# Kernel tuning notes

Measured on AMD Instinct MI355X. Metric: run time of the kernel, lower is better.

## Reference

```python
import jax, jax.numpy as jnp
import numpy as np
from math import sqrt

B, L, S, H, E, D = 2, 2048, 2048, 8, 64, 64


def setup_inputs() -> dict:
    key = jax.random.key(0)
    kq, kk, kv, kb = jax.random.split(key, 4)
    queries = jax.random.normal(kq, (B, L, H, E), dtype=jnp.float32)
    keys = jax.random.normal(kk, (B, S, H, E), dtype=jnp.float32)
    values = jax.random.normal(kv, (B, S, H, D), dtype=jnp.float32)
    # TriangularCausalMask: True above the diagonal (positions to mask)
    causal = jnp.triu(jnp.ones((L, S), dtype=bool), k=1)
    attn_mask = jnp.broadcast_to(causal[None, None], (B, 1, L, S))
    attn_bias = jax.random.normal(kb, (B, L, S, H), dtype=jnp.float32) * 0.1
    return {"queries": queries, "keys": keys, "values": values,
            "attn_mask": attn_mask, "attn_bias": attn_bias}


def reference(queries, keys, values, attn_mask, attn_bias):
    scale = 1.0 / sqrt(E)
    # scores: [B, H, L, S]
    scores = jnp.einsum('blhe,bshe->bhls', queries, keys)
    scores = jnp.where(attn_mask, -jnp.inf, scores)
    bias = jnp.transpose(attn_bias, (0, 3, 1, 2))  # [B,H,L,S]
    A = jax.nn.softmax(scores * scale + bias, axis=-1)  # dropout = identity (eval)
    V = jnp.einsum('bhls,bshd->blhd', A, values)
    return V
```

## Files before the change

kernel.cpp:

```cpp
#include <hip/hip_runtime.h>
#include <stdint.h>

#define Bb 2
#define Ll 2048
#define Ss 2048
#define Hh 8
#define Ee 64
#define Dd 64

#define LOG2E 1.4426950408889634f
#define QSCALE (0.125f * LOG2E)
#define NEG_BIG (-1e30f)
#define QT_ELEMS 2097152

typedef short bf16x8 __attribute__((ext_vector_type(8)));
typedef short bf16x4 __attribute__((ext_vector_type(4)));
typedef float f32x4  __attribute__((ext_vector_type(4)));

__device__ __forceinline__ short f2bf(float f) {
  uint32_t u = __float_as_uint(f);
  u += 0x7fffu + ((u >> 16) & 1u);
  return (short)(u >> 16);
}
__device__ __forceinline__ float bf2f(short s) {
  return __uint_as_float(((uint32_t)(unsigned short)s) << 16);
}
__device__ __forceinline__ f32x4 mfma_pv(bf16x4 a, bf16x4 b, f32x4 c) {
#if __has_builtin(__builtin_amdgcn_mfma_f32_16x16x16_bf16)
  return __builtin_amdgcn_mfma_f32_16x16x16_bf16(a, b, c, 0, 0, 0);
#else
  return __builtin_amdgcn_mfma_f32_16x16x16bf16_1k(a, b, c, 0, 0, 0);
#endif
}

#define BLOCK_SYNC() do {                                   \
    asm volatile("s_waitcnt lgkmcnt(0)" ::: "memory");      \
    __builtin_amdgcn_s_barrier();                           \
    asm volatile("" ::: "memory");                          \
  } while (0)

__global__ __launch_bounds__(256)
void prep_qkv(const float* __restrict__ Q, const float* __restrict__ K,
              const float* __restrict__ V, short* __restrict__ Qt,
              short* __restrict__ Kt, short* __restrict__ Vt)
{
  const int blk = blockIdx.x;
  const int tid = threadIdx.x;
  if (blk < 1024) {
    const int c = tid & 15;
    #pragma unroll
    for (int pass = 0; pass < 4; ++pass) {
      const int rowg = blk * 64 + pass * 16 + (tid >> 4);
      const int tensor = rowg >> 15;
      const int r2 = rowg & 32767;
      const float* src = (tensor ? K : Q) + (size_t)r2 * 64 + c * 4;
      const float4 v = *(const float4*)(src);
      const int b = r2 >> 14, l = (r2 >> 3) & 2047, hh = r2 & 7;
      const float sc = tensor ? 1.0f : QSCALE;
      bf16x4 o;
      o[0] = f2bf(v.x * sc); o[1] = f2bf(v.y * sc);
      o[2] = f2bf(v.z * sc); o[3] = f2bf(v.w * sc);
      short* dst = (tensor ? Kt : Qt) + ((size_t)((b * 8 + hh) * 2048 + l)) * 64 + c * 4;
      *reinterpret_cast<bf16x4*>(dst) = o;
    }
  } else {
    const int vb = blk - 1024;
    const int plane = vb >> 5;
    const int b = plane >> 3, hh = plane & 7;
    const int sc = (vb & 31) * 64;
    const int w = tid >> 6, d = tid & 63;
    const int sbase = sc + w * 16;
    const float* src = V + (((size_t)b * Ss + sbase) * Hh + hh) * Dd + d;
    float vals[16];
    #pragma unroll
    for (int i = 0; i < 16; ++i) vals[i] = src[(size_t)i * (Hh * Dd)];
    bf16x8 o0, o1;
    #pragma unroll
    for (int i = 0; i < 8; ++i) { o0[i] = f2bf(vals[i]); o1[i] = f2bf(vals[i + 8]); }
    short* dst = Vt + ((size_t)(plane * 64 + d)) * 2048 + sbase;
    *reinterpret_cast<bf16x8*>(dst)     = o0;
    *reinterpret_cast<bf16x8*>(dst + 8) = o1;
  }
}

__global__ __launch_bounds__(256, 1)
void fattn4(const short* __restrict__ Qt, const short* __restrict__ Kt,
            const short* __restrict__ Vt, const float* __restrict__ Bias,
            float* __restrict__ Out)
{
  __shared__ short Vs[2][4][64][72];
  __shared__ short Bs[2][4][4][16][16];

  const int tid  = threadIdx.x;
  const int wv   = tid >> 6;
  const int lane = tid & 63;
  const int g    = lane >> 4;
  const int n    = lane & 15;

  const int rid    = blockIdx.x;
  const int xcd    = rid & 7;
  const int b      = xcd >> 2;
  const int hhalf  = (xcd >> 1) & 1;
  const int z      = xcd & 1;
  const int pairid = (rid >> 3) * 2 + z;
  const int h      = hhalf * 4 + wv;
  const int p      = b * 8 + h;

  const int sl = tid >> 4;
  const int sq = tid & 15;
  const int srcb = (lane & 48) | ((lane >> 2) & 12);

  for (int job = 0; job < 2; ++job) {
    const int lg = job ? pairid : (127 - pairid);
    const int l0 = lg * 16;
    const int ntiles = (lg >> 2) + 1;
    const int lq = l0 + n;

    const short* qp = Qt + ((size_t)(p * 2048 + l0 + n)) * 64 + g * 8;
    const bf16x8 qf0 = *reinterpret_cast<const bf16x8*>(qp);
    const bf16x8 qf1 = *reinterpret_cast<const bf16x8*>(qp + 32);

    const short* kbase  = Kt + ((size_t)(p * 2048 + n)) * 64 + g * 8;
    const short* vstage = Vt + ((size_t)(p * 64 + lane)) * 2048;
    const float* gb = Bias + (((size_t)(b * Ll + l0 + sl)) * Ss + sq) * Hh + hhalf * 4;

    f32x4 acc[4];
    #pragma unroll
    for (int dt = 0; dt < 4; ++dt) { f32x4 zz = {0.f,0.f,0.f,0.f}; acc[dt] = zz; }
    float m = NEG_BIG, lsum = 0.f;

    bf16x8 kA[4][2], kB[4][2];
    float4 gB0, gB1, gB2, gB3;

#define ISSUE_K(KN, soff) do {                                              \
      const short* kp_ = kbase + (size_t)(soff) * 64;                       \
      _Pragma("unroll")                                                     \
      for (int st_ = 0; st_ < 4; ++st_) {                                   \
        KN[st_][0] = *reinterpret_cast<const bf16x8*>(kp_ + st_ * 16 * 64); \
        KN[st_][1] = *reinterpret_cast<const bf16x8*>(kp_ + st_ * 16 * 64 + 32); \
      }                                                                     \
    } while (0)

#define ISSUE_BIAS(G0, G1, G2, G3, soff) do {                               \
      const float* gp_ = gb + (size_t)(soff) * Hh;                          \
      G0 = *(const float4*)(gp_);                                           \
      G1 = *(const float4*)(gp_ + (size_t)16 * Hh);                         \
      G2 = *(const float4*)(gp_ + (size_t)32 * Hh);                         \
      G3 = *(const float4*)(gp_ + (size_t)48 * Hh);                         \
    } while (0)

#define WRITE_BIAS(buf, G0, G1, G2, G3) do {                                \
      short* w0_ = &Bs[buf][0][0][sl][sq];                                  \
      short* w1_ = &Bs[buf][0][1][sl][sq];                                  \
      short* w2_ = &Bs[buf][0][2][sl][sq];                                  \
      short* w3_ = &Bs[buf][0][3][sl][sq];                                  \
      w0_[0]=f2bf(G0.x*LOG2E); w0_[1024]=f2bf(G0.y*LOG2E); w0_[2048]=f2bf(G0.z*LOG2E); w0_[3072]=f2bf(G0.w*LOG2E); \
      w1_[0]=f2bf(G1.x*LOG2E); w1_[1024]=f2bf(G1.y*LOG2E); w1_[2048]=f2bf(G1.z*LOG2E); w1_[3072]=f2bf(G1.w*LOG2E); \
      w2_[0]=f2bf(G2.x*LOG2E); w2_[1024]=f2bf(G2.y*LOG2E); w2_[2048]=f2bf(G2.z*LOG2E); w2_[3072]=f2bf(G2.w*LOG2E); \
      w3_[0]=f2bf(G3.x*LOG2E); w3_[1024]=f2bf(G3.y*LOG2E); w3_[2048]=f2bf(G3.z*LOG2E); w3_[3072]=f2bf(G3.w*LOG2E); \
    } while (0)

    {
      float4 a0, a1, a2, a3;
      ISSUE_BIAS(a0, a1, a2, a3, 0);
      ISSUE_BIAS(gB0, gB1, gB2, gB3, 64);
      ISSUE_K(kA, 0);
      bf16x8 v0[8];
      #pragma unroll
      for (int c = 0; c < 8; ++c)
        v0[c] = *reinterpret_cast<const bf16x8*>(vstage + c * 8);
      WRITE_BIAS(0, a0, a1, a2, a3);
      #pragma unroll
      for (int c = 0; c < 8; ++c)
        *reinterpret_cast<bf16x8*>(&Vs[0][wv][lane][c * 8]) = v0[c];
    }
    BLOCK_SYNC();

#define TILE(KC, KN, t) do {                                                \
      const int s0_ = (t) * 64;                                             \
      const int cb_ = (t) & 1, nb_ = cb_ ^ 1;                               \
      const bool more1_ = ((t) + 1 < ntiles);                               \
      const bool more2_ = ((t) + 2 < ntiles);                               \
       \
      if (more1_) ISSUE_K(KN, s0_ + 64);                                    \
      bf16x8 vN_[8];                                                        \
      if (more1_) {                                                         \
        _Pragma("unroll")                                                   \
        for (int c = 0; c < 8; ++c)                                         \
          vN_[c] = *reinterpret_cast<const bf16x8*>(vstage + s0_ + 64 + c * 8); \
      }                                                                     \
                                                    \
      f32x4 sacc_[4];                                                       \
      _Pragma("unroll")                                                     \
      for (int st_ = 0; st_ < 4; ++st_) {                                   \
        const bf16x4 bb_ = *reinterpret_cast<const bf16x4*>(&Bs[cb_][wv][st_][n][4 * g]); \
        f32x4 zz_ = {0.f, 0.f, 0.f, 0.f};                                   \
        f32x4 sv_ = __builtin_amdgcn_mfma_f32_16x16x32_bf16(KC[st_][0], qf0, zz_, 0, 0, 0); \
        sv_ = __builtin_amdgcn_mfma_f32_16x16x32_bf16(KC[st_][1], qf1, sv_, 0, 0, 0); \
        const int sb_ = s0_ + st_ * 16 + 4 * g;                             \
        _Pragma("unroll")                                                   \
        for (int r_ = 0; r_ < 4; ++r_)                                      \
          sacc_[st_][r_] = (sb_ + r_ <= lq) ? (sv_[r_] + bf2f(bb_[r_])) : NEG_BIG; \
      }                                                                     \
                                            \
      float tm_ = NEG_BIG;                                                  \
      _Pragma("unroll")                                                     \
      for (int st_ = 0; st_ < 4; ++st_)                                     \
        _Pragma("unroll")                                                   \
        for (int r_ = 0; r_ < 4; ++r_) tm_ = fmaxf(tm_, sacc_[st_][r_]);    \
      tm_ = fmaxf(tm_, __shfl_xor(tm_, 16));                                \
      tm_ = fmaxf(tm_, __shfl_xor(tm_, 32));                                \
      if (__any(tm_ - m > 8.f)) {                                           \
        const float mn_ = fmaxf(m, tm_);                                    \
        const float corr_ = exp2f(m - mn_);                                 \
        m = mn_; lsum *= corr_;                                             \
        const float c0_ = __shfl(corr_, srcb);                              \
        const float c1_ = __shfl(corr_, srcb + 1);                          \
        const float c2_ = __shfl(corr_, srcb + 2);                          \
        const float c3_ = __shfl(corr_, srcb + 3);                          \
        _Pragma("unroll")                                                   \
        for (int dt_ = 0; dt_ < 4; ++dt_) {                                 \
          acc[dt_][0] *= c0_; acc[dt_][1] *= c1_;                           \
          acc[dt_][2] *= c2_; acc[dt_][3] *= c3_;                           \
        }                                                                   \
      }                                                                     \
      bf16x4 pa_[4];                                                        \
      float ps_ = 0.f;                                                      \
      _Pragma("unroll")                                                     \
      for (int st_ = 0; st_ < 4; ++st_) {                                   \
        _Pragma("unroll")                                                   \
        for (int r_ = 0; r_ < 4; ++r_) {                                    \
          const float pe_ = exp2f(sacc_[st_][r_] - m);                      \
          ps_ += pe_;                                                       \
          pa_[st_][r_] = f2bf(pe_);                                         \
        }                                                                   \
      }                                                                     \
      ps_ += __shfl_xor(ps_, 16);                                           \
      ps_ += __shfl_xor(ps_, 32);                                           \
      lsum += ps_;                                                          \
                       \
      _Pragma("unroll")                                                     \
      for (int st_ = 0; st_ < 4; ++st_) {                                   \
        _Pragma("unroll")                                                   \
        for (int dt_ = 0; dt_ < 4; ++dt_) {                                 \
          const bf16x4 vb_ = *reinterpret_cast<const bf16x4*>(              \
              &Vs[cb_][wv][dt_ * 16 + n][st_ * 16 + 4 * g]);                \
          acc[dt_] = mfma_pv(pa_[st_], vb_, acc[dt_]);                      \
        }                                                                   \
      }                                                                     \
                                  \
      if (more1_) {                                                         \
        _Pragma("unroll")                                                   \
        for (int c = 0; c < 8; ++c)                                         \
          *reinterpret_cast<bf16x8*>(&Vs[nb_][wv][lane][c * 8]) = vN_[c];   \
        WRITE_BIAS(nb_, gB0, gB1, gB2, gB3);                                \
      }                                                                     \
      if (more2_) ISSUE_BIAS(gB0, gB1, gB2, gB3, s0_ + 128);                \
      BLOCK_SYNC();                                                         \
    } while (0)

    int t = 0;
    for (;;) {
      TILE(kA, kB, t); if (++t == ntiles) break;
      TILE(kB, kA, t); if (++t == ntiles) break;
    }

    const float i0 = 1.0f / __shfl(lsum, srcb);
    const float i1 = 1.0f / __shfl(lsum, srcb + 1);
    const float i2 = 1.0f / __shfl(lsum, srcb + 2);
    const float i3 = 1.0f / __shfl(lsum, srcb + 3);
    float* ob = Out + ((size_t)((b * Ll + l0 + 4 * g) * Hh + h)) * Dd + n;
    #pragma unroll
    for (int dt = 0; dt < 4; ++dt) {
      ob[0 * Hh * Dd + dt * 16] = acc[dt][0] * i0;
      ob[1 * Hh * Dd + dt * 16] = acc[dt][1] * i1;
      ob[2 * Hh * Dd + dt * 16] = acc[dt][2] * i2;
      ob[3 * Hh * Dd + dt * 16] = acc[dt][3] * i3;
    }

#undef TILE
#undef WRITE_BIAS
#undef ISSUE_BIAS
#undef ISSUE_K
  }
}

extern "C" void kernel_launch(void* const* d_in, const int* in_sizes, int n_in,
                              void* d_out, int out_size, void* d_ws, size_t ws_size,
                              hipStream_t stream) {
  const float* Q    = (const float*)d_in[0];
  const float* K    = (const float*)d_in[1];
  const float* V    = (const float*)d_in[2];
  const float* Bias = (const float*)d_in[4];
  float* Out = (float*)d_out;

  short* wsp = (short*)d_ws;
  short* Qt = wsp;
  short* Kt = wsp + QT_ELEMS;
  short* Vt = wsp + 2 * (size_t)QT_ELEMS;

  prep_qkv<<<dim3(1536), dim3(256), 0, stream>>>(Q, K, V, Qt, Kt, Vt);
  fattn4<<<dim3(256), dim3(256), 0, stream>>>(Qt, Kt, Vt, Bias, Out);
}
```

Measured before the change: 100.7 us.

## Drop V LDS staging, split paired jobs into separate blocks, allow two blocks per CU

The V tile is no longer staged through shared memory. Each lane now loads its bf16x4 MFMA operands straight from global Vt, which removes the V LDS buffer and its store and read traffic. The two-job pairing loop per block becomes one query tile per block, with twice as many blocks launched, heaviest tiles first. Launch bounds change from one to two blocks per CU to raise occupancy. In exchange, V is read with many small strided global loads rather than coalesced bf16x8 loads, and the per-block causal load balancing from pairing short and long rows is lost.

```diff
diff --git a/kernel.cpp b/kernel.cpp
--- a/kernel.cpp
+++ b/kernel.cpp
@@ -83,12 +83,11 @@
   }
 }
 
-__global__ __launch_bounds__(256, 1)
-void fattn4(const short* __restrict__ Qt, const short* __restrict__ Kt,
+__global__ __launch_bounds__(256, 2)
+void fattn5(const short* __restrict__ Qt, const short* __restrict__ Kt,
             const short* __restrict__ Vt, const float* __restrict__ Bias,
             float* __restrict__ Out)
 {
-  __shared__ short Vs[2][4][64][72];
   __shared__ short Bs[2][4][4][16][16];
 
   const int tid  = threadIdx.x;
@@ -97,192 +96,175 @@
   const int g    = lane >> 4;
   const int n    = lane & 15;
 
-  const int rid    = blockIdx.x;
-  const int xcd    = rid & 7;
-  const int b      = xcd >> 2;
-  const int hhalf  = (xcd >> 1) & 1;
-  const int z      = xcd & 1;
-  const int pairid = (rid >> 3) * 2 + z;
-  const int h      = hhalf * 4 + wv;
-  const int p      = b * 8 + h;
+  const int rid   = blockIdx.x;
+  const int xcd   = rid & 7;
+  const int b     = xcd >> 2;
+  const int hhalf = (xcd >> 1) & 1;
+  const int zz    = xcd & 1;
+  const int ord   = rid >> 3;
+  const int lg    = 2 * (63 - ord) + zz;
+  const int l0    = lg * 16;
+  const int ntiles = (lg >> 2) + 1;
+  const int h     = hhalf * 4 + wv;
+  const int p     = b * 8 + h;
+  const int lq    = l0 + n;
 
   const int sl = tid >> 4;
   const int sq = tid & 15;
   const int srcb = (lane & 48) | ((lane >> 2) & 12);
 
-  for (int job = 0; job < 2; ++job) {
-    const int lg = job ? pairid : (127 - pairid);
-    const int l0 = lg * 16;
-    const int ntiles = (lg >> 2) + 1;
-    const int lq = l0 + n;
-
-    const short* qp = Qt + ((size_t)(p * 2048 + l0 + n)) * 64 + g * 8;
-    const bf16x8 qf0 = *reinterpret_cast<const bf16x8*>(qp);
-    const bf16x8 qf1 = *reinterpret_cast<const bf16x8*>(qp + 32);
-
-    const short* kbase  = Kt + ((size_t)(p * 2048 + n)) * 64 + g * 8;
-    const short* vstage = Vt + ((size_t)(p * 64 + lane)) * 2048;
-    const float* gb = Bias + (((size_t)(b * Ll + l0 + sl)) * Ss + sq) * Hh + hhalf * 4;
-
-    f32x4 acc[4];
-    #pragma unroll
-    for (int dt = 0; dt < 4; ++dt) { f32x4 zz = {0.f,0.f,0.f,0.f}; acc[dt] = zz; }
-    float m = NEG_BIG, lsum = 0.f;
-
-    bf16x8 kA[4][2], kB[4][2];
-    float4 gB0, gB1, gB2, gB3;
+  const short* qp = Qt + ((size_t)(p * 2048 + l0 + n)) * 64 + g * 8;
+  const bf16x8 qf0 = *reinterpret_cast<const bf16x8*>(qp);
+  const bf16x8 qf1 = *reinterpret_cast<const bf16x8*>(qp + 32);
+
+  const short* kbase = Kt + ((size_t)(p * 2048 + n)) * 64 + g * 8;
+  const short* vbase = Vt + ((size_t)(p * 64 + n)) * 2048 + 4 * g;
+  const float* gb = Bias + (((size_t)(b * Ll + l0 + sl)) * Ss + sq) * Hh + hhalf * 4;
+
+  f32x4 acc[4];
+  #pragma unroll
+  for (int dt = 0; dt < 4; ++dt) { f32x4 z = {0.f,0.f,0.f,0.f}; acc[dt] = z; }
+  float m = NEG_BIG, lsum = 0.f;
+
+  bf16x8 kA[4][2], kB[4][2];
+  float4 gB0, gB1, gB2, gB3;
 
 #define ISSUE_K(KN, soff) do {                                              \
-      const short* kp_ = kbase + (size_t)(soff) * 64;                       \
-      _Pragma("unroll")                                                     \
-      for (int st_ = 0; st_ < 4; ++st_) {                                   \
-        KN[st_][0] = *reinterpret_cast<const bf16x8*>(kp_ + st_ * 16 * 64); \
-        KN[st_][1] = *reinterpret_cast<const bf16x8*>(kp_ + st_ * 16 * 64 + 32); \
+    const short* kp_ = kbase + (size_t)(soff) * 64;                         \
+    _Pragma("unroll")                                                       \
+    for (int st_ = 0; st_ < 4; ++st_) {                                     \
+      KN[st_][0] = *reinterpret_cast<const bf16x8*>(kp_ + st_ * 16 * 64);   \
+      KN[st_][1] = *reinterpret_cast<const bf16x8*>(kp_ + st_ * 16 * 64 + 32); \
+    }                                                                       \
+  } while (0)
+
+#define ISSUE_BIAS(G0, G1, G2, G3, soff) do {                               \
+    const float* gp_ = gb + (size_t)(soff) * Hh;                            \
+    G0 = *(const float4*)(gp_);                                             \
+    G1 = *(const float4*)(gp_ + (size_t)16 * Hh);                           \
+    G2 = *(const float4*)(gp_ + (size_t)32 * Hh);                           \
+    G3 = *(const float4*)(gp_ + (size_t)48 * Hh);                           \
+  } while (0)
+
+#define WRITE_BIAS(buf, G0, G1, G2, G3) do {                                \
+    short* w0_ = &Bs[buf][0][0][sl][sq];                                    \
+    short* w1_ = &Bs[buf][0][1][sl][sq];                                    \
+    short* w2_ = &Bs[buf][0][2][sl][sq];                                    \
+    short* w3_ = &Bs[buf][0][3][sl][sq];                                    \
+    w0_[0]=f2bf(G0.x*LOG2E); w0_[1024]=f2bf(G0.y*LOG2E); w0_[2048]=f2bf(G0.z*LOG2E); w0_[3072]=f2bf(G0.w*LOG2E); \
+    w1_[0]=f2bf(G1.x*LOG2E); w1_[1024]=f2bf(G1.y*LOG2E); w1_[2048]=f2bf(G1.z*LOG2E); w1_[3072]=f2bf(G1.w*LOG2E); \
+    w2_[0]=f2bf(G2.x*LOG2E); w2_[1024]=f2bf(G2.y*LOG2E); w2_[2048]=f2bf(G2.z*LOG2E); w2_[3072]=f2bf(G2.w*LOG2E); \
+    w3_[0]=f2bf(G3.x*LOG2E); w3_[1024]=f2bf(G3.y*LOG2E); w3_[2048]=f2bf(G3.z*LOG2E); w3_[3072]=f2bf(G3.w*LOG2E); \
+  } while (0)
+
+  {
+    float4 a0, a1, a2, a3;
+    ISSUE_BIAS(a0, a1, a2, a3, 0);
+    ISSUE_BIAS(gB0, gB1, gB2, gB3, 64);
+    ISSUE_K(kA, 0);
+    WRITE_BIAS(0, a0, a1, a2, a3);
+  }
+  BLOCK_SYNC();
+
+#define TILE(KC, KN, t) do {                                                \
+    const int s0_ = (t) * 64;                                               \
+    const int cb_ = (t) & 1, nb_ = cb_ ^ 1;                                 \
+    const bool more1_ = ((t) + 1 < ntiles);                                 \
+    const bool more2_ = ((t) + 2 < ntiles);                                 \
+       \
+    if (more1_) ISSUE_K(KN, s0_ + 64);                                      \
+    bf16x4 vb_[4][4];                                                       \
+    _Pragma("unroll")                                                       \
+    for (int st_ = 0; st_ < 4; ++st_)                                       \
+      _Pragma("unroll")                                                     \
+      for (int dt_ = 0; dt_ < 4; ++dt_)                                     \
+        vb_[st_][dt_] = *reinterpret_cast<const bf16x4*>(                   \
+            vbase + (size_t)dt_ * 16 * 2048 + s0_ + st_ * 16);              \
+                                                    \
+    f32x4 sacc_[4];                                                         \
+    _Pragma("unroll")                                                       \
+    for (int st_ = 0; st_ < 4; ++st_) {                                     \
+      const bf16x4 bb_ = *reinterpret_cast<const bf16x4*>(&Bs[cb_][wv][st_][n][4 * g]); \
+      f32x4 zz_ = {0.f, 0.f, 0.f, 0.f};                                     \
+      f32x4 sv_ = __builtin_amdgcn_mfma_f32_16x16x32_bf16(KC[st_][0], qf0, zz_, 0, 0, 0); \
+      sv_ = __builtin_amdgcn_mfma_f32_16x16x32_bf16(KC[st_][1], qf1, sv_, 0, 0, 0); \
+      const int sb_ = s0_ + st_ * 16 + 4 * g;                               \
+      _Pragma("unroll")                                                     \
+      for (int r_ = 0; r_ < 4; ++r_)                                        \
+        sacc_[st_][r_] = (sb_ + r_ <= lq) ? (sv_[r_] + bf2f(bb_[r_])) : NEG_BIG; \
+    }                                                                       \
+                                            \
+    float tm_ = NEG_BIG;                                                    \
+    _Pragma("unroll")                                                       \
+    for (int st_ = 0; st_ < 4; ++st_)                                       \
+      _Pragma("unroll")                                                     \
+      for (int r_ = 0; r_ < 4; ++r_) tm_ = fmaxf(tm_, sacc_[st_][r_]);      \
+    tm_ = fmaxf(tm_, __shfl_xor(tm_, 16));                                  \
+    tm_ = fmaxf(tm_, __shfl_xor(tm_, 32));                                  \
+    if (__any(tm_ - m > 8.f)) {                                             \
+      const float mn_ = fmaxf(m, tm_);                                      \
+      const float corr_ = exp2f(m - mn_);                                   \
+      m = mn_; lsum *= corr_;                                               \
+      const float c0_ = __shfl(corr_, srcb);                                \
+      const float c1_ = __shfl(corr_, srcb + 1);                            \
+      const float c2_ = __shfl(corr_, srcb + 2);                            \
+      const float c3_ = __shfl(corr_, srcb + 3);                            \
+      _Pragma("unroll")                                                     \
+      for (int dt_ = 0; dt_ < 4; ++dt_) {                                   \
+        acc[dt_][0] *= c0_; acc[dt_][1] *= c1_;                             \
+        acc[dt_][2] *= c2_; acc[dt_][3] *= c3_;                             \
       }                                                                     \
-    } while (0)
-
-#define ISSUE_BIAS(G0, G1, G2, G3, soff) do {                               \
-      const float* gp_ = gb + (size_t)(soff) * Hh;                          \
-      G0 = *(const float4*)(gp_);                                           \
-      G1 = *(const float4*)(gp_ + (size_t)16 * Hh);                         \
-      G2 = *(const float4*)(gp_ + (size_t)32 * Hh);                         \
-      G3 = *(const float4*)(gp_ + (size_t)48 * Hh);                         \
-    } while (0)
-
-#define WRITE_BIAS(buf, G0, G1, G2, G3) do {                                \
-      short* w0_ = &Bs[buf][0][0][sl][sq];                                  \
-      short* w1_ = &Bs[buf][0][1][sl][sq];                                  \
-      short* w2_ = &Bs[buf][0][2][sl][sq];                                  \
-      short* w3_ = &Bs[buf][0][3][sl][sq];                                  \
-      w0_[0]=f2bf(G0.x*LOG2E); w0_[1024]=f2bf(G0.y*LOG2E); w0_[2048]=f2bf(G0.z*LOG2E); w0_[3072]=f2bf(G0.w*LOG2E); \
-      w1_[0]=f2bf(G1.x*LOG2E); w1_[1024]=f2bf(G1.y*LOG2E); w1_[2048]=f2bf(G1.z*LOG2E); w1_[3072]=f2bf(G1.w*LOG2E); \
-      w2_[0]=f2bf(G2.x*LOG2E); w2_[1024]=f2bf(G2.y*LOG2E); w2_[2048]=f2bf(G2.z*LOG2E); w2_[3072]=f2bf(G2.w*LOG2E); \
-      w3_[0]=f2bf(G3.x*LOG2E); w3_[1024]=f2bf(G3.y*LOG2E); w3_[2048]=f2bf(G3.z*LOG2E); w3_[3072]=f2bf(G3.w*LOG2E); \
-    } while (0)
-
-    {
-      float4 a0, a1, a2, a3;
-      ISSUE_BIAS(a0, a1, a2, a3, 0);
-      ISSUE_BIAS(gB0, gB1, gB2, gB3, 64);
-      ISSUE_K(kA, 0);
-      bf16x8 v0[8];
-      #pragma unroll
-      for (int c = 0; c < 8; ++c)
-        v0[c] = *reinterpret_cast<const bf16x8*>(vstage + c * 8);
-      WRITE_BIAS(0, a0, a1, a2, a3);
-      #pragma unroll
-      for (int c = 0; c < 8; ++c)
-        *reinterpret_cast<bf16x8*>(&Vs[0][wv][lane][c * 8]) = v0[c];
-    }
-    BLOCK_SYNC();
-
-#define TILE(KC, KN, t) do {                                                \
-      const int s0_ = (t) * 64;                                             \
-      const int cb_ = (t) & 1, nb_ = cb_ ^ 1;                               \
-      const bool more1_ = ((t) + 1 < ntiles);                               \
-      const bool more2_ = ((t) + 2 < ntiles);                               \
-       \
-      if (more1_) ISSUE_K(KN, s0_ + 64);                                    \
-      bf16x8 vN_[8];                                                        \
-      if (more1_) {                                                         \
-        _Pragma("unroll")                                                   \
-        for (int c = 0; c < 8; ++c)                                         \
-          vN_[c] = *reinterpret_cast<const bf16x8*>(vstage + s0_ + 64 + c * 8); \
+    }                                                                       \
+    bf16x4 pa_[4];                                                          \
+    float ps_ = 0.f;                                                        \
+    _Pragma("unroll")                                                       \
+    for (int st_ = 0; st_ < 4; ++st_) {                                     \
+      _Pragma("unroll")                                                     \
+      for (int r_ = 0; r_ < 4; ++r_) {                                      \
+        const float pe_ = exp2f(sacc_[st_][r_] - m);                        \
+        ps_ += pe_;                                                         \
+        pa_[st_][r_] = f2bf(pe_);                                           \
       }                                                                     \
-                                                    \
-      f32x4 sacc_[4];                                                       \
-      _Pragma("unroll")                                                     \
-      for (int st_ = 0; st_ < 4; ++st_) {                                   \
-        const bf16x4 bb_ = *reinterpret_cast<const bf16x4*>(&Bs[cb_][wv][st_][n][4 * g]); \
-        f32x4 zz_ = {0.f, 0.f, 0.f, 0.f};                                   \
-        f32x4 sv_ = __builtin_amdgcn_mfma_f32_16x16x32_bf16(KC[st_][0], qf0, zz_, 0, 0, 0); \
-        sv_ = __builtin_amdgcn_mfma_f32_16x16x32_bf16(KC[st_][1], qf1, sv_, 0, 0, 0); \
-        const int sb_ = s0_ + st_ * 16 + 4 * g;                             \
-        _Pragma("unroll")                                                   \
-        for (int r_ = 0; r_ < 4; ++r_)                                      \
-          sacc_[st_][r_] = (sb_ + r_ <= lq) ? (sv_[r_] + bf2f(bb_[r_])) : NEG_BIG; \
-      }                                                                     \
-                                            \
-      float tm_ = NEG_BIG;                                                  \
-      _Pragma("unroll")                                                     \
-      for (int st_ = 0; st_ < 4; ++st_)                                     \
-        _Pragma("unroll")                                                   \
-        for (int r_ = 0; r_ < 4; ++r_) tm_ = fmaxf(tm_, sacc_[st_][r_]);    \
-      tm_ = fmaxf(tm_, __shfl_xor(tm_, 16));                                \
-      tm_ = fmaxf(tm_, __shfl_xor(tm_, 32));                                \
-      if (__any(tm_ - m > 8.f)) {                                           \
-        const float mn_ = fmaxf(m, tm_);                                    \
-        const float corr_ = exp2f(m - mn_);                                 \
-        m = mn_; lsum *= corr_;                                             \
-        const float c0_ = __shfl(corr_, srcb);                              \
-        const float c1_ = __shfl(corr_, srcb + 1);                          \
-        const float c2_ = __shfl(corr_, srcb + 2);                          \
-        const float c3_ = __shfl(corr_, srcb + 3);                          \
-        _Pragma("unroll")                                                   \
-        for (int dt_ = 0; dt_ < 4; ++dt_) {                                 \
-          acc[dt_][0] *= c0_; acc[dt_][1] *= c1_;                           \
-          acc[dt_][2] *= c2_; acc[dt_][3] *= c3_;                           \
-        }                                                                   \
-      }                                                                     \
-      bf16x4 pa_[4];                                                        \
-      float ps_ = 0.f;                                                      \
-      _Pragma("unroll")                                                     \
-      for (int st_ = 0; st_ < 4; ++st_) {                                   \
-        _Pragma("unroll")                                                   \
-        for (int r_ = 0; r_ < 4; ++r_) {                                    \
-          const float pe_ = exp2f(sacc_[st_][r_] - m);                      \
-          ps_ += pe_;                                                       \
-          pa_[st_][r_] = f2bf(pe_);                                         \
-        }                                                                   \
-      }                                                                     \
-      ps_ += __shfl_xor(ps_, 16);                                           \
-      ps_ += __shfl_xor(ps_, 32);                                           \
-      lsum += ps_;                                                          \
-                       \
-      _Pragma("unroll")                                                     \
-      for (int st_ = 0; st_ < 4; ++st_) {                                   \
-        _Pragma("unroll")                                                   \
-        for (int dt_ = 0; dt_ < 4; ++dt_) {                                 \
-          const bf16x4 vb_ = *reinterpret_cast<const bf16x4*>(              \
-              &Vs[cb_][wv][dt_ * 16 + n][st_ * 16 + 4 * g]);                \
-          acc[dt_] = mfma_pv(pa_[st_], vb_, acc[dt_]);                      \
-        }                                                                   \
-      }                                                                     \
-                                  \
-      if (more1_) {                                                         \
-        _Pragma("unroll")                                                   \
-        for (int c = 0; c < 8; ++c)                                         \
-          *reinterpret_cast<bf16x8*>(&Vs[nb_][wv][lane][c * 8]) = vN_[c];   \
-        WRITE_BIAS(nb_, gB0, gB1, gB2, gB3);                                \
-      }                                                                     \
-      if (more2_) ISSUE_BIAS(gB0, gB1, gB2, gB3, s0_ + 128);                \
-      BLOCK_SYNC();                                                         \
-    } while (0)
-
-    int t = 0;
-    for (;;) {
-      TILE(kA, kB, t); if (++t == ntiles) break;
-      TILE(kB, kA, t); if (++t == ntiles) break;
-    }
-
-    const float i0 = 1.0f / __shfl(lsum, srcb);
-    const float i1 = 1.0f / __shfl(lsum, srcb + 1);
-    const float i2 = 1.0f / __shfl(lsum, srcb + 2);
-    const float i3 = 1.0f / __shfl(lsum, srcb + 3);
-    float* ob = Out + ((size_t)((b * Ll + l0 + 4 * g) * Hh + h)) * Dd + n;
-    #pragma unroll
-    for (int dt = 0; dt < 4; ++dt) {
-      ob[0 * Hh * Dd + dt * 16] = acc[dt][0] * i0;
-      ob[1 * Hh * Dd + dt * 16] = acc[dt][1] * i1;
-      ob[2 * Hh * Dd + dt * 16] = acc[dt][2] * i2;
-      ob[3 * Hh * Dd + dt * 16] = acc[dt][3] * i3;
-    }
+    }                                                                       \
+    ps_ += __shfl_xor(ps_, 16);                                             \
+    ps_ += __shfl_xor(ps_, 32);                                             \
+    lsum += ps_;                                                            \
+         \
+    _Pragma("unroll")                                                       \
+    for (int st_ = 0; st_ < 4; ++st_) {                                     \
+      _Pragma("unroll")                                                     \
+      for (int dt_ = 0; dt_ < 4; ++dt_)                                     \
+        acc[dt_] = mfma_pv(pa_[st_], vb_[st_][dt_], acc[dt_]);              \
+    }                                                                       \
+                           \
+    if (more1_) WRITE_BIAS(nb_, gB0, gB1, gB2, gB3);                        \
+    if (more2_) ISSUE_BIAS(gB0, gB1, gB2, gB3, s0_ + 128);                  \
+    BLOCK_SYNC();                                                           \
+  } while (0)
+
+  int t = 0;
+  for (;;) {
+    TILE(kA, kB, t); if (++t == ntiles) break;
+    TILE(kB, kA, t); if (++t == ntiles) break;
+  }
+
+  const float i0 = 1.0f / __shfl(lsum, srcb);
+  const float i1 = 1.0f / __shfl(lsum, srcb + 1);
+  const float i2 = 1.0f / __shfl(lsum, srcb + 2);
+  const float i3 = 1.0f / __shfl(lsum, srcb + 3);
+  float* ob = Out + ((size_t)((b * Ll + l0 + 4 * g) * Hh + h)) * Dd + n;
+  #pragma unroll
+  for (int dt = 0; dt < 4; ++dt) {
+    ob[0 * Hh * Dd + dt * 16] = acc[dt][0] * i0;
+    ob[1 * Hh * Dd + dt * 16] = acc[dt][1] * i1;
+    ob[2 * Hh * Dd + dt * 16] = acc[dt][2] * i2;
+    ob[3 * Hh * Dd + dt * 16] = acc[dt][3] * i3;
+  }
 
 #undef TILE
 #undef WRITE_BIAS
 #undef ISSUE_BIAS
 #undef ISSUE_K
-  }
 }
 
 extern "C" void kernel_launch(void* const* d_in, const int* in_sizes, int n_in,
@@ -300,5 +282,5 @@
   short* Vt = wsp + 2 * (size_t)QT_ELEMS;
 
   prep_qkv<<<dim3(1536), dim3(256), 0, stream>>>(Q, K, V, Qt, Kt, Vt);
-  fattn4<<<dim3(256), dim3(256), 0, stream>>>(Qt, Kt, Vt, Bias, Out);
-}
+  fattn5<<<dim3(512), dim3(256), 0, stream>>>(Qt, Kt, Vt, Bias, Out);
+}
```

Result: slower. 155.0 us (+54.0%).
